# Kernel tuning notes

Measured on AMD Instinct MI355X. Metric: run time of the kernel, lower is better.

The kernel has to match this reference:

```python
import jax, jax.numpy as jnp
import numpy as np

CE_TEMP = 1.0
SIMW_TEMP = 0.1
NSEG = 2048
EPS = 1e-8
NEG = jnp.float32(-1e30)


def setup_inputs() -> dict:
    key = jax.random.key(0)
    k1, k2, k3, k4, k5, k6 = jax.random.split(key, 6)
    N, C, H, W, Ch, S = 2, 19, 128, 128, 256, NSEG
    inputs_plbl = jax.random.normal(k1, (N, C, H, W), dtype=jnp.float32)
    feats_plbl = jax.random.normal(k2, (N, Ch, H, W), dtype=jnp.float32)
    inputs = jax.random.normal(k3, (N, C, H, W), dtype=jnp.float32)
    # multi-hot targets per superpixel; ~2.3 active classes on average -> many multi-hot rows
    targets = jax.random.bernoulli(k4, 0.12, (N, S, C)).astype(jnp.float32)
    superpixels = jax.random.randint(k5, (N, H, W), 0, S, dtype=jnp.int32)
    spmasks = jax.random.bernoulli(k6, 0.5, (N, H, W))
    return {"inputs_plbl": inputs_plbl, "feats_plbl": feats_plbl, "inputs": inputs,
            "targets": targets, "superpixels": superpixels, "spmasks": spmasks}


def _per_image(out_plbl, feat, out, trg_table, sp, mask):
    # out_plbl: [HW,C] softmax'd pseudo-label probs; feat: [HW,Ch]; out: [HW,C];
    # trg_table: [S,C] multi-hot; sp: [HW] int superpixel ids; mask: [HW] bool
    HW, C = out_plbl.shape
    S = trg_table.shape[0]
    trg_pix = trg_table[sp]                                  # [HW,C]
    multi_spx = trg_table.sum(-1) > 1.0                      # [S]
    valid = mask & multi_spx[sp]                             # == spmask & multi-hot mask

    # scatter_max: argmax pixel per (superpixel, class) among valid pixels
    scores = jnp.where(valid[:, None], out_plbl, NEG)
    seg_max = jax.ops.segment_max(scores, sp, num_segments=S)       # [S,C]
    is_max = valid[:, None] & (scores >= seg_max[sp])
    cand = jnp.where(is_max, jnp.arange(HW, dtype=jnp.int32)[:, None], HW)
    proto_idx = jax.ops.segment_min(cand, sp, num_segments=S)       # [S,C]
    proto_idx = jnp.clip(proto_idx, 0, HW - 1)

    # prototype features and per-pixel similarities to own-superpixel class prototypes
    proto_feat = feat[proto_idx]                             # [S,C,Ch]
    pf_pix = proto_feat[sp]                                  # [HW,C,Ch] (dominant intermediate)
    sim = jnp.einsum('kcd,kd->kc', pf_pix, feat) / SIMW_TEMP  # [HW,C]

    # scatter_softmax over the active classes of the pixel's superpixel
    active = trg_pix > 0.0
    w_multi = jax.nn.softmax(jnp.where(active, sim, NEG), axis=-1)
    w_row = jnp.where(active, w_multi, trg_pix)              # inactive entries keep 0
    w = jnp.where(valid[:, None], w_row, trg_pix)            # non-multi pixels keep one-hot
    w = jax.lax.stop_gradient(w)                             # original computes weights under no_grad

    ce = -jnp.log(out + EPS)                                 # [HW,C]
    contrib = jnp.where(mask[:, None], w * ce, 0.0)
    any_valid = jnp.any(valid)                               # image skipped if no multi-hot masked pixel
    loss_i = jnp.where(any_valid, contrib.sum(), 0.0)
    cnt_i = jnp.where(any_valid, mask.sum(), 0)
    return loss_i, cnt_i


def reference(inputs_plbl, feats_plbl, inputs, targets, superpixels, spmasks):
    N, C, H, W = inputs_plbl.shape
    Ch = feats_plbl.shape[1]
    out_plbl = jax.nn.softmax(inputs_plbl / CE_TEMP, axis=1).transpose(0, 2, 3, 1).reshape(N, -1, C)
    feats = feats_plbl.transpose(0, 2, 3, 1).reshape(N, -1, Ch)
    out = jax.nn.softmax(inputs / CE_TEMP, axis=1).transpose(0, 2, 3, 1).reshape(N, -1, C)
    sp = superpixels.reshape(N, -1)
    mask = spmasks.reshape(N, -1)
    loss_i, cnt_i = jax.vmap(_per_image)(out_plbl, feats, out, targets, sp, mask)
    total = loss_i.sum()
    cnt = cnt_i.sum()
    return jnp.where(cnt > 0, total / jnp.maximum(cnt, 1).astype(jnp.float32), 0.0)
```

## Files before the change

### kernel.cpp

```cpp
#include <hip/hip_runtime.h>
#include <cstdint>
#include <cstddef>

#define NN   2
#define CC   19
#define HWD  16384
#define CH   256
#define SS   2048
#define BCAP 32

#define EPSV 1e-8f

#define MAIN_BLKS  (2 * NN * HWD / 256)
#define TRAN_BLKS  ((HWD / 64) * (CH / 64) * NN)

__global__ __launch_bounds__(256) void k_fused(
        const float* __restrict__ xp, const float* __restrict__ xi,
        const float* __restrict__ F, const float* __restrict__ trg,
        const int* __restrict__ sp, const int* __restrict__ msk,
        int* __restrict__ sp_cnt, unsigned short* __restrict__ bucket,
        float* __restrict__ plbl_pm, float* __restrict__ ce_pm,
        float* __restrict__ feat_t, int* __restrict__ cnt,
        int* __restrict__ vcnt, float* __restrict__ slots) {
    __shared__ float tile[64][65];
    __shared__ unsigned char vld[64];

    if (blockIdx.x < MAIN_BLKS) {
        int gid = blockIdx.x * blockDim.x + threadIdx.x;
        int partB = (gid >= NN * HWD);
        int idx = partB ? gid - NN * HWD : gid;
        int n = idx >> 14;
        int k = idx & (HWD - 1);
        int lane = threadIdx.x & 63;
        int m = (msk[idx] != 0);
        int s = sp[idx];
        const float* t = trg + ((size_t)n * SS + s) * CC;
        int mu = 0;
        if (m) {
            float ts = 0.f;
            #pragma unroll
            for (int c = 0; c < CC; ++c) ts += t[c];
            mu = (ts > 1.0f);
        }
        int valid = m && mu;

        if (!partB) {
            unsigned long long mb = __ballot(m);
            unsigned long long vb = __ballot(valid);
            if (valid) {
                int cell = n * SS + s;
                int pos = atomicAdd(&sp_cnt[cell], 1);
                if (pos < BCAP) bucket[(size_t)cell * BCAP + pos] = (unsigned short)k;
                const float* a = xp + (size_t)n * CC * HWD + k;
                float v[CC];
                float mx = -1e30f;
                #pragma unroll
                for (int c = 0; c < CC; ++c) { v[c] = a[(size_t)c * HWD]; mx = fmaxf(mx, v[c]); }
                float su = 0.f;
                #pragma unroll
                for (int c = 0; c < CC; ++c) { v[c] = expf(v[c] - mx); su += v[c]; }
                float inv = 1.f / su;
                float* op = plbl_pm + (size_t)idx * CC;
                #pragma unroll
                for (int c = 0; c < CC; ++c) op[c] = v[c] * inv;
            }
            if (lane == 0) {
                if (mb) atomicAdd(&cnt[n], __popcll(mb));
                if (vb) atomicAdd(&vcnt[n], __popcll(vb));
            }
        } else {
            float contrib = 0.f;
            if (m) {
                const float* b = xi + (size_t)n * CC * HWD + k;
                float v[CC];
                float mx = -1e30f;
                #pragma unroll
                for (int c = 0; c < CC; ++c) { v[c] = b[(size_t)c * HWD]; mx = fmaxf(mx, v[c]); }
                float su = 0.f;
                #pragma unroll
                for (int c = 0; c < CC; ++c) { v[c] = expf(v[c] - mx); su += v[c]; }
                float inv = 1.f / su;
                if (mu) {
                    float* cp = ce_pm + (size_t)idx * CC;
                    #pragma unroll
                    for (int c = 0; c < CC; ++c) cp[c] = -logf(v[c] * inv + EPSV);
                } else {
                    #pragma unroll
                    for (int c = 0; c < CC; ++c) contrib += t[c] * (-logf(v[c] * inv + EPSV));
                }
            }
            #pragma unroll
            for (int off = 32; off >= 1; off >>= 1) contrib += __shfl_xor(contrib, off);
            if (lane == 0 && contrib != 0.f)
                atomicAdd(&slots[n * 128 + ((idx >> 6) & 127)], contrib);
        }
    } else {
        int b2 = blockIdx.x - MAIN_BLKS;
        int k0 = (b2 & 255) * 64;
        int d0 = ((b2 >> 8) & 3) * 64;
        int n  = b2 >> 10;
        int tx = threadIdx.x & 63, ty = threadIdx.x >> 6;
        const float* src = F + (size_t)n * CH * HWD;
        float* dst = feat_t + (size_t)n * HWD * CH;

        if (ty == 0) {
            int pix = n * HWD + k0 + tx;
            int m = (msk[pix] != 0);
            int flag = 0;
            if (m) {
                int s = sp[pix];
                const float* t = trg + ((size_t)n * SS + s) * CC;
                float ts = 0.f;
                #pragma unroll
                for (int c = 0; c < CC; ++c) ts += t[c];
                flag = (ts > 1.0f);
            }
            vld[tx] = (unsigned char)flag;
        }
        #pragma unroll
        for (int i = 0; i < 16; ++i) {
            int dd = ty + 4 * i;
            tile[dd][tx] = src[(size_t)(d0 + dd) * HWD + (k0 + tx)];
        }
        __syncthreads();
        #pragma unroll
        for (int i = 0; i < 16; ++i) {
            int kk = ty + 4 * i;
            if (vld[kk]) dst[(size_t)(k0 + kk) * CH + (d0 + tx)] = tile[tx][kk];
        }
    }
}

__global__ __launch_bounds__(256) void k_sim(
        const float* __restrict__ feat_t, const float* __restrict__ ce_pm,
        const float* __restrict__ plbl_pm, const float* __restrict__ trg,
        const int* __restrict__ sp_cnt, const unsigned short* __restrict__ bucket,
        float* __restrict__ slots) {
    int id = blockIdx.x;
    int cnt_c = sp_cnt[id];
    if (cnt_c == 0) return;
    cnt_c = min(cnt_c, BCAP);
    int n    = id >> 11;
    int tid  = threadIdx.x;
    int lane = tid & 63;
    int wv   = tid >> 6;

    __shared__ float protoF[CC][CH];
    __shared__ float s_bv[4][CC];
    __shared__ int   s_bi[4][CC];
    __shared__ int   s_proto[CC];
    __shared__ int   actc[CC];

    float t = (lane < CC) ? trg[(size_t)id * CC + lane] : 0.f;
    unsigned long long act = __ballot(t > 0.f);
    int nact = __popcll(act);
    int apos = __popcll(act & ((1ull << lane) - 1ull));
    if ((act >> lane) & 1ull) actc[apos] = lane;
    int mypix = (lane < cnt_c) ? (int)bucket[(size_t)id * BCAP + lane] : 0;

    float bv = -1e30f;
    int   bi = HWD;
    for (int i = wv; i < cnt_c; i += 4) {
        int pix = __shfl(mypix, i);
        if (lane < CC) {
            float v = plbl_pm[((size_t)(n * HWD + pix)) * CC + lane];
            if (v > bv || (v == bv && pix < bi)) { bv = v; bi = pix; }
        }
    }
    if (lane < CC) { s_bv[wv][lane] = bv; s_bi[wv][lane] = bi; }
    __syncthreads();
    if (lane < CC) {
        bv = -1e30f; bi = HWD;
        #pragma unroll
        for (int j = 0; j < 4; ++j) {
            float v = s_bv[j][lane];
            int   p = s_bi[j][lane];
            if (v > bv || (v == bv && p < bi)) { bv = v; bi = p; }
        }
        if ((act >> lane) & 1ull) s_proto[apos] = bi;
    }
    __syncthreads();

    for (int a = wv; a < nact; a += 4) {
        int p = s_proto[a];
        ((float4*)(&protoF[a][0]))[lane] =
            ((const float4*)(feat_t + ((size_t)(n * HWD + p)) * CH))[lane];
    }
    __syncthreads();

    float wcontrib = 0.f;
    for (int i = wv; i < cnt_c; i += 4) {
        int pix = __shfl(mypix, i);
        float ce = (lane < nact)
                 ? ce_pm[((size_t)(n * HWD + pix)) * CC + actc[lane]] : 0.f;
        float4 f = ((const float4*)(feat_t + ((size_t)(n * HWD + pix)) * CH))[lane];
        float mysim = -1e30f;
        for (int a = 0; a < nact; ++a) {
            float4 pf = ((const float4*)(&protoF[a][0]))[lane];
            float d = f.x * pf.x + f.y * pf.y + f.z * pf.z + f.w * pf.w;
            #pragma unroll
            for (int off = 32; off >= 1; off >>= 1) d += __shfl_xor(d, off);
            if (lane == a) mysim = d * 10.0f;
        }
        float mx = mysim;
        #pragma unroll
        for (int off = 32; off >= 1; off >>= 1) mx = fmaxf(mx, __shfl_xor(mx, off));
        float e = (lane < nact) ? expf(mysim - mx) : 0.f;
        float se = e;
        #pragma unroll
        for (int off = 32; off >= 1; off >>= 1) se += __shfl_xor(se, off);
        float c1 = (e / se) * ce;
        #pragma unroll
        for (int off = 32; off >= 1; off >>= 1) c1 += __shfl_xor(c1, off);
        wcontrib += c1;
    }
    if (lane == 0 && wcontrib != 0.f)
        atomicAdd(&slots[n * 128 + (id & 127)], wcontrib);
}

__global__ void k_final(const float* __restrict__ slots, const int* __restrict__ cnt,
                        const int* __restrict__ vcnt, float* __restrict__ out) {
    __shared__ float red[2];
    int t = threadIdx.x;
    int w = t >> 6;
    int lane = t & 63;
    float v = slots[w * 128 + lane] + slots[w * 128 + lane + 64];
    #pragma unroll
    for (int off = 32; off >= 1; off >>= 1) v += __shfl_xor(v, off);
    if (lane == 0) red[w] = v;
    __syncthreads();
    if (t == 0) {
        float total = 0.f;
        int c = 0;
        for (int n = 0; n < NN; ++n)
            if (vcnt[n] > 0) { total += red[n]; c += cnt[n]; }
        out[0] = (c > 0) ? total / (float)c : 0.f;
    }
}

extern "C" void kernel_launch(void* const* d_in, const int* in_sizes, int n_in,
                              void* d_out, int out_size, void* d_ws, size_t ws_size,
                              hipStream_t stream) {
    const float* inputs_plbl = (const float*)d_in[0];
    const float* feats_plbl  = (const float*)d_in[1];
    const float* inputs      = (const float*)d_in[2];
    const float* targets     = (const float*)d_in[3];
    const int*   superpixels = (const int*)d_in[4];
    const int*   spmasks     = (const int*)d_in[5];
    float* out = (float*)d_out;

    char* ws = (char*)d_ws;
    int*   sp_cnt = (int*)ws;
    int*   cnt    = (int*)(ws + 16384);
    int*   vcnt   = (int*)(ws + 16392);
    float* slots  = (float*)(ws + 16416);
    unsigned short* bucket = (unsigned short*)(ws + 17440);
    float* plbl_pm = (float*)(ws + 279584);
    float* ce_pm   = (float*)(ws + 2769952);
    float* feat_t  = (float*)(ws + 5260320);

    hipMemsetAsync(ws, 0, 17440, stream);

    k_fused<<<MAIN_BLKS + TRAN_BLKS, 256, 0, stream>>>(
        inputs_plbl, inputs, feats_plbl, targets, superpixels, spmasks,
        sp_cnt, bucket, plbl_pm, ce_pm, feat_t, cnt, vcnt, slots);
    k_sim<<<NN * SS, 256, 0, stream>>>(feat_t, ce_pm, plbl_pm, targets,
                                       sp_cnt, bucket, slots);
    k_final<<<1, 128, 0, stream>>>(slots, cnt, vcnt, out);
}
```

Baseline: 128.9 us.

## Store transposed features as bf16 and compute CE via log-softmax

```diff
diff --git a/kernel.cpp b/kernel.cpp
--- a/kernel.cpp
+++ b/kernel.cpp
@@ -9,10 +9,16 @@
 #define SS   2048
 #define BCAP 32
 
-#define EPSV 1e-8f
-
 #define MAIN_BLKS  (2 * NN * HWD / 256)
 #define TRAN_BLKS  ((HWD / 64) * (CH / 64) * NN)
+
+__device__ __forceinline__ unsigned short f2bf(float x) {
+    unsigned u = __float_as_uint(x);
+    return (unsigned short)((u + 0x7FFFu + ((u >> 16) & 1u)) >> 16);
+}
+__device__ __forceinline__ float bf2f(unsigned short h) {
+    return __uint_as_float(((unsigned)h) << 16);
+}
 
 __global__ __launch_bounds__(256) void k_fused(
         const float* __restrict__ xp, const float* __restrict__ xi,
@@ -20,7 +26,7 @@
         const int* __restrict__ sp, const int* __restrict__ msk,
         int* __restrict__ sp_cnt, unsigned short* __restrict__ bucket,
         float* __restrict__ plbl_pm, float* __restrict__ ce_pm,
-        float* __restrict__ feat_t, int* __restrict__ cnt,
+        unsigned short* __restrict__ feat_t, int* __restrict__ cnt,
         int* __restrict__ vcnt, float* __restrict__ slots) {
     __shared__ float tile[64][65];
     __shared__ unsigned char vld[64];
@@ -78,15 +84,15 @@
                 for (int c = 0; c < CC; ++c) { v[c] = b[(size_t)c * HWD]; mx = fmaxf(mx, v[c]); }
                 float su = 0.f;
                 #pragma unroll
-                for (int c = 0; c < CC; ++c) { v[c] = expf(v[c] - mx); su += v[c]; }
-                float inv = 1.f / su;
+                for (int c = 0; c < CC; ++c) su += expf(v[c] - mx);
+                float lsu = logf(su);
                 if (mu) {
                     float* cp = ce_pm + (size_t)idx * CC;
                     #pragma unroll
-                    for (int c = 0; c < CC; ++c) cp[c] = -logf(v[c] * inv + EPSV);
+                    for (int c = 0; c < CC; ++c) cp[c] = lsu - (v[c] - mx);
                 } else {
                     #pragma unroll
-                    for (int c = 0; c < CC; ++c) contrib += t[c] * (-logf(v[c] * inv + EPSV));
+                    for (int c = 0; c < CC; ++c) contrib += t[c] * (lsu - (v[c] - mx));
                 }
             }
             #pragma unroll
@@ -101,7 +107,7 @@
         int n  = b2 >> 10;
         int tx = threadIdx.x & 63, ty = threadIdx.x >> 6;
         const float* src = F + (size_t)n * CH * HWD;
-        float* dst = feat_t + (size_t)n * HWD * CH;
+        unsigned short* dst = feat_t + (size_t)n * HWD * CH;
 
         if (ty == 0) {
             int pix = n * HWD + k0 + tx;
@@ -126,13 +132,13 @@
         #pragma unroll
         for (int i = 0; i < 16; ++i) {
             int kk = ty + 4 * i;
-            if (vld[kk]) dst[(size_t)(k0 + kk) * CH + (d0 + tx)] = tile[tx][kk];
+            if (vld[kk]) dst[(size_t)(k0 + kk) * CH + (d0 + tx)] = f2bf(tile[tx][kk]);
         }
     }
 }
 
 __global__ __launch_bounds__(256) void k_sim(
-        const float* __restrict__ feat_t, const float* __restrict__ ce_pm,
+        const unsigned short* __restrict__ feat_t, const float* __restrict__ ce_pm,
         const float* __restrict__ plbl_pm, const float* __restrict__ trg,
         const int* __restrict__ sp_cnt, const unsigned short* __restrict__ bucket,
         float* __restrict__ slots) {
@@ -183,8 +189,9 @@
 
     for (int a = wv; a < nact; a += 4) {
         int p = s_proto[a];
-        ((float4*)(&protoF[a][0]))[lane] =
-            ((const float4*)(feat_t + ((size_t)(n * HWD + p)) * CH))[lane];
+        ushort4 q = ((const ushort4*)(feat_t + ((size_t)(n * HWD + p)) * CH))[lane];
+        float4 v = make_float4(bf2f(q.x), bf2f(q.y), bf2f(q.z), bf2f(q.w));
+        ((float4*)(&protoF[a][0]))[lane] = v;
     }
     __syncthreads();
 
@@ -193,7 +200,8 @@
         int pix = __shfl(mypix, i);
         float ce = (lane < nact)
                  ? ce_pm[((size_t)(n * HWD + pix)) * CC + actc[lane]] : 0.f;
-        float4 f = ((const float4*)(feat_t + ((size_t)(n * HWD + pix)) * CH))[lane];
+        ushort4 q = ((const ushort4*)(feat_t + ((size_t)(n * HWD + pix)) * CH))[lane];
+        float4 f = make_float4(bf2f(q.x), bf2f(q.y), bf2f(q.z), bf2f(q.w));
         float mysim = -1e30f;
         for (int a = 0; a < nact; ++a) {
             float4 pf = ((const float4*)(&protoF[a][0]))[lane];
@@ -257,7 +265,7 @@
     unsigned short* bucket = (unsigned short*)(ws + 17440);
     float* plbl_pm = (float*)(ws + 279584);
     float* ce_pm   = (float*)(ws + 2769952);
-    float* feat_t  = (float*)(ws + 5260320);
+    unsigned short* feat_t = (unsigned short*)(ws + 5260320);
 
     hipMemsetAsync(ws, 0, 17440, stream);
 
```

New measurement: 128.4 us. No clear change (-0.4%).
